# Performance work log

Measured on AMD Instinct MI355X. Metric: run time of the kernel, lower is better.

The kernel has to match this reference:

```python
import jax, jax.numpy as jnp
import numpy as np

B, D_IN, H, LAT = 4096, 4096, 4096, 512


def setup_inputs() -> dict:
    key = jax.random.key(0)
    ks = jax.random.split(key, 10)
    s = lambda fan_in: 1.0 / np.sqrt(fan_in)
    return {
        "x": jax.random.normal(ks[0], (B, D_IN), jnp.float32),
        "W_e1": jax.random.normal(ks[1], (D_IN, H), jnp.float32) * s(D_IN),
        "b_e1": jax.random.uniform(ks[2], (H,), jnp.float32),
        "W_e2": jax.random.normal(ks[3], (H, 2 * LAT), jnp.float32) * s(H),
        "b_e2": jax.random.uniform(ks[4], (2 * LAT,), jnp.float32),
        "W_d1": jax.random.normal(ks[5], (LAT, H), jnp.float32) * s(LAT),
        "b_d1": jax.random.uniform(ks[6], (H,), jnp.float32),
        "W_d2": jax.random.normal(ks[7], (H, D_IN), jnp.float32) * s(H),
        "b_d2": jax.random.uniform(ks[8], (D_IN,), jnp.float32),
        "eps": jax.random.normal(ks[9], (B, LAT), jnp.float32),
    }


def reference(x, W_e1, b_e1, W_e2, b_e2, W_d1, b_d1, W_d2, b_d2, eps):
    # encoder MLP
    h = jax.nn.relu(x @ W_e1 + b_e1)
    z = h @ W_e2 + b_e2                      # [B, 2*LAT]
    mu, logvar = z[:, :LAT], z[:, LAT:]
    # reparameterize: cholesky(diag(exp(logvar))) @ eps + mu == exp(0.5*logvar)*eps + mu
    zs = mu + jnp.exp(0.5 * logvar) * eps    # [B, LAT]
    # decoder MLP
    hd = jax.nn.relu(zs @ W_d1 + b_d1)
    recon = hd @ W_d2 + b_d2                 # [B, D_IN]
    return recon, mu, logvar
```

## Files before the change

### kernel.cpp

```cpp
#include <hip/hip_runtime.h>
#include <hip/hip_bf16.h>

typedef __attribute__((ext_vector_type(8))) __bf16 bf16x8;
typedef __attribute__((ext_vector_type(4))) float f32x4;
typedef __attribute__((ext_vector_type(4))) unsigned short ushort4v;
typedef unsigned short u16;

__device__ __forceinline__ u16 f2bf_bits(float f) {
    union { float f; unsigned int u; } x; x.f = f;
    unsigned int r = x.u + 0x7FFFu + ((x.u >> 16) & 1u);
    return (u16)(r >> 16);
}

__device__ __forceinline__ void gload_lds16(const void* g, void* l) {
    __builtin_amdgcn_global_load_lds(
        (const __attribute__((address_space(1))) void*)g,
        (__attribute__((address_space(3))) void*)l, 16, 0, 0);
}

#define BARRIER()  __builtin_amdgcn_s_barrier()
#define LGKM0()    asm volatile("s_waitcnt lgkmcnt(0)" ::: "memory")
#define VMW8()     asm volatile("s_waitcnt vmcnt(8)" ::: "memory")

__global__ void cvt4(const float* __restrict__ in, u16* __restrict__ out, int n) {
    int i = (blockIdx.x * 256 + threadIdx.x) << 2;
    if (i >= n) return;
    f32x4 v = *reinterpret_cast<const f32x4*>(in + i);
    ushort4v o;
    o.x = f2bf_bits(v.x); o.y = f2bf_bits(v.y);
    o.z = f2bf_bits(v.z); o.w = f2bf_bits(v.w);
    *reinterpret_cast<ushort4v*>(out + i) = o;
}

__global__ __launch_bounds__(256)
void transpose_cvt64(const float* __restrict__ in, u16* __restrict__ out,
                     int R, int C) {
    __shared__ float t[64][67];
    const int c0 = blockIdx.x << 6;
    const int r0 = blockIdx.y << 6;
    const int tx = threadIdx.x & 15;
    const int ty = threadIdx.x >> 4;
    #pragma unroll
    for (int j = 0; j < 4; ++j) {
        f32x4 v = *reinterpret_cast<const f32x4*>(
            &in[(size_t)(r0 + ty + 16 * j) * C + c0 + (tx << 2)]);
        *reinterpret_cast<f32x4*>(&t[ty + 16 * j][tx << 2]) = v;
    }
    __syncthreads();
    const int oc = threadIdx.x >> 2;
    const int rr = (threadIdx.x & 3) << 2;
    #pragma unroll
    for (int j = 0; j < 4; ++j) {
        const int r = rr + 16 * j;
        ushort4v o;
        o.x = f2bf_bits(t[r + 0][oc]);
        o.y = f2bf_bits(t[r + 1][oc]);
        o.z = f2bf_bits(t[r + 2][oc]);
        o.w = f2bf_bits(t[r + 3][oc]);
        *reinterpret_cast<ushort4v*>(&out[(size_t)(c0 + oc) * R + r0 + r]) = o;
    }
}

__global__ __launch_bounds__(256)
void zred(const float* __restrict__ P, const float* __restrict__ be2,
          const float* __restrict__ eps, float* __restrict__ mu,
          float* __restrict__ lv, u16* __restrict__ zs) {
    const int i = blockIdx.x * 256 + threadIdx.x;
    const int r = i >> 7;
    const int c4 = (i & 127) << 2;
    const size_t base = (size_t)r * 1024 + c4;
    const size_t PS = (size_t)4096 * 1024;

    f32x4 m = *reinterpret_cast<const f32x4*>(P + base);
    f32x4 l = *reinterpret_cast<const f32x4*>(P + base + 512);
    #pragma unroll
    for (int s = 1; s < 4; ++s) {
        m += *reinterpret_cast<const f32x4*>(P + s * PS + base);
        l += *reinterpret_cast<const f32x4*>(P + s * PS + base + 512);
    }
    m += *reinterpret_cast<const f32x4*>(be2 + c4);
    l += *reinterpret_cast<const f32x4*>(be2 + 512 + c4);

    const size_t ob = (size_t)r * 512 + c4;
    *reinterpret_cast<f32x4*>(mu + ob) = m;
    *reinterpret_cast<f32x4*>(lv + ob) = l;

    f32x4 e = *reinterpret_cast<const f32x4*>(eps + ob);
    ushort4v o;
    o.x = f2bf_bits(m.x + __expf(0.5f * l.x) * e.x);
    o.y = f2bf_bits(m.y + __expf(0.5f * l.y) * e.y);
    o.z = f2bf_bits(m.z + __expf(0.5f * l.z) * e.z);
    o.w = f2bf_bits(m.w + __expf(0.5f * l.w) * e.w);
    *reinterpret_cast<ushort4v*>(zs + ob) = o;
}

template<int MODE>
__global__ __launch_bounds__(512, 2)
void gemm256(const u16* __restrict__ A, const u16* __restrict__ Bt,
             const float* __restrict__ bias,
             u16* __restrict__ obf, float* __restrict__ of32,
             int M, int N, int K, int ntiles)
{
    extern __shared__ char lds[];
    const int tid  = threadIdx.x;
    const int lane = tid & 63;
    const int w    = tid >> 6;
    const int wr   = w >> 2;
    const int wc   = w & 3;

    int bid = blockIdx.x;
    int sid = 0;
    int nwg = gridDim.x;
    if (MODE == 3) { sid = bid & 3; bid >>= 2; nwg >>= 2; }
    const int cpx = nwg >> 3;
    bid = (bid & 7) * cpx + (bid >> 3);
    const int nbx  = N >> 8;
    const int brow = (bid / nbx) << 8;
    const int bcol = (bid % nbx) << 8;
    const int kbase = (MODE == 3) ? sid * ntiles : 0;
    float* pout = (MODE == 3) ? of32 + (size_t)sid * M * N : of32;

    const int srow  = tid >> 3;
    const int scole = (((tid & 7) ^ (srow & 7)) << 4) >> 1;
    const size_t aoff = (size_t)(brow + srow) * K + scole;
    const size_t boff = (size_t)(bcol + srow) * K + scole;
    const size_t rowK64 = (size_t)64 * K;
    const int wave1024 = w << 10;

    const int lo16 = (lane >> 4) << 4;
    const int swzm = (lane & 7) << 4;
    const int low0 = lo16 ^ swzm;
    const int low1 = (64 | lo16) ^ swzm;
    const int rA   = (lane & 15) << 7;
    const int rB   = ((((wc & 1) << 6) | (lane & 15)) << 7);
    const int regA = wr << 14;
    const int regB = 32768 + ((wc >> 1) << 14);

    bf16x8 a[4][2];
    bf16x8 b0[2][2];
    bf16x8 b1[2][2];
    f32x4 acc[8][4];
    #pragma unroll
    for (int m = 0; m < 8; ++m)
        #pragma unroll
        for (int n = 0; n < 4; ++n)
            acc[m][n] = (f32x4)(0.0f);

#define STAGE_A(buf, h, kt) do { \
    const u16* _s = A + aoff + (size_t)(h) * 128 * K + (size_t)(kt) * 64; \
    gload_lds16(_s,          lds + ((buf) << 16) + ((h) << 14) + wave1024); \
    gload_lds16(_s + rowK64, lds + ((buf) << 16) + ((h) << 14) + 8192 + wave1024); \
} while (0)

#define STAGE_B(buf, h, kt) do { \
    const u16* _s = Bt + boff + (size_t)(h) * 128 * K + (size_t)(kt) * 64; \
    gload_lds16(_s,          lds + ((buf) << 16) + 32768 + ((h) << 14) + wave1024); \
    gload_lds16(_s + rowK64, lds + ((buf) << 16) + 32768 + ((h) << 14) + 8192 + wave1024); \
} while (0)

#define READ_A(buf, g) do { \
    _Pragma("unroll") \
    for (int m = 0; m < 4; ++m) { \
        const int _b = ((buf) << 16) + regA + rA + ((((g) << 2) + m) << 11); \
        a[m][0] = *reinterpret_cast<const bf16x8*>(lds + _b + low0); \
        a[m][1] = *reinterpret_cast<const bf16x8*>(lds + _b + low1); \
    } \
} while (0)

#define READ_B0(buf) do { \
    _Pragma("unroll") \
    for (int n = 0; n < 2; ++n) { \
        const int _b = ((buf) << 16) + regB + rB + (n << 11); \
        b0[n][0] = *reinterpret_cast<const bf16x8*>(lds + _b + low0); \
        b0[n][1] = *reinterpret_cast<const bf16x8*>(lds + _b + low1); \
    } \
} while (0)

#define READ_B1(buf) do { \
    _Pragma("unroll") \
    for (int n = 0; n < 2; ++n) { \
        const int _b = ((buf) << 16) + regB + rB + ((n + 2) << 11); \
        b1[n][0] = *reinterpret_cast<const bf16x8*>(lds + _b + low0); \
        b1[n][1] = *reinterpret_cast<const bf16x8*>(lds + _b + low1); \
    } \
} while (0)

#define MM(bx, mb, nb) do { \
    __builtin_amdgcn_s_setprio(1); \
    _Pragma("unroll") \
    for (int m = 0; m < 4; ++m) \
        _Pragma("unroll") \
        for (int n = 0; n < 2; ++n) \
            _Pragma("unroll") \
            for (int s = 0; s < 2; ++s) \
                acc[(mb) + m][(nb) + n] = __builtin_amdgcn_mfma_f32_16x16x32_bf16( \
                    a[m][s], bx[n][s], acc[(mb) + m][(nb) + n], 0, 0, 0); \
    __builtin_amdgcn_s_setprio(0); \
} while (0)

    const int NIT = ntiles >> 1;

    STAGE_A(0, 0, kbase); STAGE_A(0, 1, kbase); STAGE_B(0, 0, kbase); STAGE_B(0, 1, kbase);
    STAGE_A(1, 0, kbase + 1); STAGE_A(1, 1, kbase + 1); STAGE_B(1, 0, kbase + 1); STAGE_B(1, 1, kbase + 1);
    VMW8(); BARRIER();
    READ_A(0, 0); READ_B0(0);

    for (int it = 0; it < NIT; ++it) {
        const int tn0r = 2 * it + 2;
        const int tn1r = 2 * it + 3;
        const int tn0 = kbase + (tn0r < ntiles ? tn0r : ntiles - 1);
        const int tn1 = kbase + (tn1r < ntiles ? tn1r : ntiles - 1);

        BARRIER(); LGKM0();
        MM(b0, 0, 0);
        READ_B1(0);

        BARRIER(); LGKM0();
        STAGE_B(0, 0, tn0);
        MM(b1, 0, 2);
        READ_A(0, 1);

        BARRIER(); LGKM0();
        STAGE_B(0, 1, tn0);
        MM(b1, 4, 2);

        BARRIER(); LGKM0();
        STAGE_A(0, 0, tn0); STAGE_A(0, 1, tn0);
        MM(b0, 4, 0);
        VMW8();
        READ_A(1, 0); READ_B0(1);

        BARRIER(); LGKM0();
        MM(b0, 0, 0);
        READ_B1(1);

        BARRIER(); LGKM0();
        STAGE_B(1, 0, tn1);
        MM(b1, 0, 2);
        READ_A(1, 1);

        BARRIER(); LGKM0();
        STAGE_B(1, 1, tn1);
        MM(b1, 4, 2);

        BARRIER(); LGKM0();
        STAGE_A(1, 0, tn1); STAGE_A(1, 1, tn1);
        MM(b0, 4, 0);
        VMW8();
        READ_A(0, 0); READ_B0(0);
    }

    float bb[4];
    #pragma unroll
    for (int n = 0; n < 4; ++n)
        bb[n] = (MODE == 3) ? 0.0f : bias[bcol + (wc << 6) + (n << 4) + (lane & 15)];

    const int erow0 = brow + (wr << 7) + ((lane >> 4) << 2);
    const int ecol0 = bcol + (wc << 6) + (lane & 15);

    #pragma unroll
    for (int m = 0; m < 8; ++m) {
        #pragma unroll
        for (int i = 0; i < 4; ++i) {
            const int r = erow0 + (m << 4) + i;
            #pragma unroll
            for (int n = 0; n < 4; ++n) {
                const int c = ecol0 + (n << 4);
                float v = acc[m][n][i] + bb[n];
                if (MODE == 0) {
                    v = v > 0.0f ? v : 0.0f;
                    obf[(size_t)r * N + c] = f2bf_bits(v);
                } else {
                    pout[(size_t)r * N + c] = v;
                }
            }
        }
    }
#undef STAGE_A
#undef STAGE_B
#undef READ_A
#undef READ_B0
#undef READ_B1
#undef MM
}

extern "C" void kernel_launch(void* const* d_in, const int* in_sizes, int n_in,
                              void* d_out, int out_size, void* d_ws, size_t ws_size,
                              hipStream_t stream) {
    const float* x   = (const float*)d_in[0];
    const float* We1 = (const float*)d_in[1];
    const float* be1 = (const float*)d_in[2];
    const float* We2 = (const float*)d_in[3];
    const float* be2 = (const float*)d_in[4];
    const float* Wd1 = (const float*)d_in[5];
    const float* bd1 = (const float*)d_in[6];
    const float* Wd2 = (const float*)d_in[7];
    const float* bd2 = (const float*)d_in[8];
    const float* eps = (const float*)d_in[9];

    const int B = 4096, D = 4096, H = 4096, LAT = 512;

    char* ws = (char*)d_ws;
    u16*   xb   = (u16*)(ws);
    u16*   w1t  = (u16*)(ws + 33554432);
    u16*   w2t  = (u16*)(ws + 67108864);
    u16*   w3t  = (u16*)(ws + 75497472);
    u16*   w4t  = (u16*)(ws + 79691776);
    u16*   h    = (u16*)(ws + 113246208);
    float* part = (float*)(ws);
    u16*   zs   = (u16*)(ws + 113246208);
    u16*   hd   = (u16*)(ws);

    float* recon = (float*)d_out;
    float* mu    = recon + (size_t)B * D;
    float* lv    = mu + (size_t)B * LAT;

    hipFuncSetAttribute(reinterpret_cast<const void*>(gemm256<0>),
                        hipFuncAttributeMaxDynamicSharedMemorySize, 131072);
    hipFuncSetAttribute(reinterpret_cast<const void*>(gemm256<1>),
                        hipFuncAttributeMaxDynamicSharedMemorySize, 131072);
    hipFuncSetAttribute(reinterpret_cast<const void*>(gemm256<3>),
                        hipFuncAttributeMaxDynamicSharedMemorySize, 131072);

    cvt4<<<(B * D / 4 + 255) / 256, 256, 0, stream>>>(x, xb, B * D);
    transpose_cvt64<<<dim3(H / 64, D / 64), 256, 0, stream>>>(We1, w1t, D, H);
    transpose_cvt64<<<dim3(2 * LAT / 64, H / 64), 256, 0, stream>>>(We2, w2t, H, 2 * LAT);
    transpose_cvt64<<<dim3(H / 64, LAT / 64), 256, 0, stream>>>(Wd1, w3t, LAT, H);
    transpose_cvt64<<<dim3(D / 64, H / 64), 256, 0, stream>>>(Wd2, w4t, H, D);

    gemm256<0><<<(B / 256) * (H / 256), 512, 131072, stream>>>(
        xb, w1t, be1, h, nullptr, B, H, D, D / 64);
    gemm256<3><<<(B / 256) * (2 * LAT / 256) * 4, 512, 131072, stream>>>(
        h, w2t, nullptr, nullptr, part, B, 2 * LAT, H, (H / 64) / 4);
    zred<<<(B * LAT / 4) / 256, 256, 0, stream>>>(part, be2, eps, mu, lv, zs);
    gemm256<0><<<(B / 256) * (H / 256), 512, 131072, stream>>>(
        zs, w3t, bd1, hd, nullptr, B, H, LAT, LAT / 64);
    gemm256<1><<<(B / 256) * (D / 256), 512, 131072, stream>>>(
        hd, w4t, bd2, nullptr, recon, B, D, H, H / 64);
}
```

Measured before the change: 371.9 us.

## Switch GEMM core to 32x32x16 MFMA and widen transpose stores

Replaces the 16x16x32 bf16 MFMA tiling with 32x32x16 MFMA, which changes the LDS fragment read layout, the accumulator shape and the epilogue row/column mapping. Larger MFMA tiles reuse each operand fragment across more output, which cuts LDS read traffic and instruction count per FLOP. The transpose-convert kernel also now writes 16-byte bf16 vectors instead of 8-byte ones. The cost is a different LDS bank access pattern and larger per-instruction latency that the existing schedule must hide.

```diff
diff --git a/kernel.cpp b/kernel.cpp
--- a/kernel.cpp
+++ b/kernel.cpp
@@ -3,7 +3,9 @@
 
 typedef __attribute__((ext_vector_type(8))) __bf16 bf16x8;
 typedef __attribute__((ext_vector_type(4))) float f32x4;
+typedef __attribute__((ext_vector_type(16))) float f32x16;
 typedef __attribute__((ext_vector_type(4))) unsigned short ushort4v;
+typedef __attribute__((ext_vector_type(8))) unsigned short ushort8v;
 typedef unsigned short u16;
 
 __device__ __forceinline__ u16 f2bf_bits(float f) {
@@ -47,17 +49,16 @@
         *reinterpret_cast<f32x4*>(&t[ty + 16 * j][tx << 2]) = v;
     }
     __syncthreads();
-    const int oc = threadIdx.x >> 2;
-    const int rr = (threadIdx.x & 3) << 2;
-    #pragma unroll
-    for (int j = 0; j < 4; ++j) {
-        const int r = rr + 16 * j;
-        ushort4v o;
-        o.x = f2bf_bits(t[r + 0][oc]);
-        o.y = f2bf_bits(t[r + 1][oc]);
-        o.z = f2bf_bits(t[r + 2][oc]);
-        o.w = f2bf_bits(t[r + 3][oc]);
-        *reinterpret_cast<ushort4v*>(&out[(size_t)(c0 + oc) * R + r0 + r]) = o;
+    const int orow8 = threadIdx.x >> 3;
+    const int seg8  = (threadIdx.x & 7) << 3;
+    #pragma unroll
+    for (int p = 0; p < 2; ++p) {
+        const int oc = orow8 + (p << 5);
+        ushort8v o;
+        #pragma unroll
+        for (int i = 0; i < 8; ++i)
+            o[i] = f2bf_bits(t[seg8 + i][oc]);
+        *reinterpret_cast<ushort8v*>(&out[(size_t)(c0 + oc) * R + r0 + seg8]) = o;
     }
 }
 
@@ -127,24 +128,22 @@
     const size_t rowK64 = (size_t)64 * K;
     const int wave1024 = w << 10;
 
-    const int lo16 = (lane >> 4) << 4;
     const int swzm = (lane & 7) << 4;
-    const int low0 = lo16 ^ swzm;
-    const int low1 = (64 | lo16) ^ swzm;
-    const int rA   = (lane & 15) << 7;
-    const int rB   = ((((wc & 1) << 6) | (lane & 15)) << 7);
+    const int kA   = (lane >> 5) << 4;
+    const int rA32 = (lane & 31) << 7;
     const int regA = wr << 14;
     const int regB = 32768 + ((wc >> 1) << 14);
-
-    bf16x8 a[4][2];
-    bf16x8 b0[2][2];
-    bf16x8 b1[2][2];
-    f32x4 acc[8][4];
-    #pragma unroll
-    for (int m = 0; m < 8; ++m)
+    const int rB32 = (wc & 1) << 13;
+
+    bf16x8 aa[2][4];
+    bf16x8 b0f[4];
+    bf16x8 b1f[4];
+    f32x16 acc[4][2];
+    #pragma unroll
+    for (int mt = 0; mt < 4; ++mt)
         #pragma unroll
-        for (int n = 0; n < 4; ++n)
-            acc[m][n] = (f32x4)(0.0f);
+        for (int nt = 0; nt < 2; ++nt)
+            acc[mt][nt] = (f32x16)(0.0f);
 
 #define STAGE_A(buf, h, kt) do { \
     const u16* _s = A + aoff + (size_t)(h) * 128 * K + (size_t)(kt) * 64; \
@@ -158,43 +157,33 @@
     gload_lds16(_s + rowK64, lds + ((buf) << 16) + 32768 + ((h) << 14) + 8192 + wave1024); \
 } while (0)
 
-#define READ_A(buf, g) do { \
+#define READ_A32(buf, g) do { \
     _Pragma("unroll") \
-    for (int m = 0; m < 4; ++m) { \
-        const int _b = ((buf) << 16) + regA + rA + ((((g) << 2) + m) << 11); \
-        a[m][0] = *reinterpret_cast<const bf16x8*>(lds + _b + low0); \
-        a[m][1] = *reinterpret_cast<const bf16x8*>(lds + _b + low1); \
+    for (int mt = 0; mt < 2; ++mt) { \
+        const int _b = ((buf) << 16) + regA + ((((g) << 1) + mt) << 12) + rA32; \
+        _Pragma("unroll") \
+        for (int s = 0; s < 4; ++s) \
+            aa[mt][s] = *reinterpret_cast<const bf16x8*>( \
+                lds + _b + ((((s) << 5) | kA) ^ swzm)); \
     } \
 } while (0)
 
-#define READ_B0(buf) do { \
+#define READ_B32(buf, bf, nt) do { \
+    const int _b = ((buf) << 16) + regB + rB32 + ((nt) << 12) + ((lane & 31) << 7); \
     _Pragma("unroll") \
-    for (int n = 0; n < 2; ++n) { \
-        const int _b = ((buf) << 16) + regB + rB + (n << 11); \
-        b0[n][0] = *reinterpret_cast<const bf16x8*>(lds + _b + low0); \
-        b0[n][1] = *reinterpret_cast<const bf16x8*>(lds + _b + low1); \
-    } \
-} while (0)
-
-#define READ_B1(buf) do { \
-    _Pragma("unroll") \
-    for (int n = 0; n < 2; ++n) { \
-        const int _b = ((buf) << 16) + regB + rB + ((n + 2) << 11); \
-        b1[n][0] = *reinterpret_cast<const bf16x8*>(lds + _b + low0); \
-        b1[n][1] = *reinterpret_cast<const bf16x8*>(lds + _b + low1); \
-    } \
-} while (0)
-
-#define MM(bx, mb, nb) do { \
+    for (int s = 0; s < 4; ++s) \
+        bf[s] = *reinterpret_cast<const bf16x8*>( \
+            lds + _b + ((((s) << 5) | kA) ^ swzm)); \
+} while (0)
+
+#define MM32(bf, g, nt) do { \
     __builtin_amdgcn_s_setprio(1); \
     _Pragma("unroll") \
-    for (int m = 0; m < 4; ++m) \
+    for (int s = 0; s < 4; ++s) \
         _Pragma("unroll") \
-        for (int n = 0; n < 2; ++n) \
-            _Pragma("unroll") \
-            for (int s = 0; s < 2; ++s) \
-                acc[(mb) + m][(nb) + n] = __builtin_amdgcn_mfma_f32_16x16x32_bf16( \
-                    a[m][s], bx[n][s], acc[(mb) + m][(nb) + n], 0, 0, 0); \
+        for (int mt = 0; mt < 2; ++mt) \
+            acc[((g) << 1) + mt][nt] = __builtin_amdgcn_mfma_f32_32x32x16_bf16( \
+                aa[mt][s], bf[s], acc[((g) << 1) + mt][nt], 0, 0, 0); \
     __builtin_amdgcn_s_setprio(0); \
 } while (0)
 
@@ -203,7 +192,7 @@
     STAGE_A(0, 0, kbase); STAGE_A(0, 1, kbase); STAGE_B(0, 0, kbase); STAGE_B(0, 1, kbase);
     STAGE_A(1, 0, kbase + 1); STAGE_A(1, 1, kbase + 1); STAGE_B(1, 0, kbase + 1); STAGE_B(1, 1, kbase + 1);
     VMW8(); BARRIER();
-    READ_A(0, 0); READ_B0(0);
+    READ_A32(0, 0); READ_B32(0, b0f, 0);
 
     for (int it = 0; it < NIT; ++it) {
         const int tn0r = 2 * it + 2;
@@ -212,76 +201,76 @@
         const int tn1 = kbase + (tn1r < ntiles ? tn1r : ntiles - 1);
 
         BARRIER(); LGKM0();
-        MM(b0, 0, 0);
-        READ_B1(0);
+        MM32(b0f, 0, 0);
+        READ_B32(0, b1f, 1);
 
         BARRIER(); LGKM0();
         STAGE_B(0, 0, tn0);
-        MM(b1, 0, 2);
-        READ_A(0, 1);
+        MM32(b1f, 0, 1);
+        READ_A32(0, 1);
 
         BARRIER(); LGKM0();
         STAGE_B(0, 1, tn0);
-        MM(b1, 4, 2);
+        MM32(b1f, 1, 1);
 
         BARRIER(); LGKM0();
         STAGE_A(0, 0, tn0); STAGE_A(0, 1, tn0);
-        MM(b0, 4, 0);
+        MM32(b0f, 1, 0);
         VMW8();
-        READ_A(1, 0); READ_B0(1);
-
-        BARRIER(); LGKM0();
-        MM(b0, 0, 0);
-        READ_B1(1);
+        READ_A32(1, 0); READ_B32(1, b0f, 0);
+
+        BARRIER(); LGKM0();
+        MM32(b0f, 0, 0);
+        READ_B32(1, b1f, 1);
 
         BARRIER(); LGKM0();
         STAGE_B(1, 0, tn1);
-        MM(b1, 0, 2);
-        READ_A(1, 1);
+        MM32(b1f, 0, 1);
+        READ_A32(1, 1);
 
         BARRIER(); LGKM0();
         STAGE_B(1, 1, tn1);
-        MM(b1, 4, 2);
+        MM32(b1f, 1, 1);
 
         BARRIER(); LGKM0();
         STAGE_A(1, 0, tn1); STAGE_A(1, 1, tn1);
-        MM(b0, 4, 0);
+        MM32(b0f, 1, 0);
         VMW8();
-        READ_A(0, 0); READ_B0(0);
-    }
-
-    float bb[4];
-    #pragma unroll
-    for (int n = 0; n < 4; ++n)
-        bb[n] = (MODE == 3) ? 0.0f : bias[bcol + (wc << 6) + (n << 4) + (lane & 15)];
-
-    const int erow0 = brow + (wr << 7) + ((lane >> 4) << 2);
-    const int ecol0 = bcol + (wc << 6) + (lane & 15);
-
-    #pragma unroll
-    for (int m = 0; m < 8; ++m) {
+        READ_A32(0, 0); READ_B32(0, b0f, 0);
+    }
+
+    float bb2[2];
+    #pragma unroll
+    for (int nt = 0; nt < 2; ++nt)
+        bb2[nt] = (MODE == 3) ? 0.0f
+                              : bias[bcol + (wc << 6) + (nt << 5) + (lane & 31)];
+
+    const int erow = brow + (wr << 7) + ((lane >> 5) << 2);
+    const int ecol = bcol + (wc << 6) + (lane & 31);
+
+    #pragma unroll
+    for (int mt = 0; mt < 4; ++mt) {
         #pragma unroll
-        for (int i = 0; i < 4; ++i) {
-            const int r = erow0 + (m << 4) + i;
+        for (int r = 0; r < 16; ++r) {
+            const int row = erow + (mt << 5) + (r & 3) + ((r >> 2) << 3);
             #pragma unroll
-            for (int n = 0; n < 4; ++n) {
-                const int c = ecol0 + (n << 4);
-                float v = acc[m][n][i] + bb[n];
+            for (int nt = 0; nt < 2; ++nt) {
+                const int c = ecol + (nt << 5);
+                float v = acc[mt][nt][r] + bb2[nt];
                 if (MODE == 0) {
                     v = v > 0.0f ? v : 0.0f;
-                    obf[(size_t)r * N + c] = f2bf_bits(v);
+                    obf[(size_t)row * N + c] = f2bf_bits(v);
                 } else {
-                    pout[(size_t)r * N + c] = v;
+                    pout[(size_t)row * N + c] = v;
                 }
             }
         }
     }
 #undef STAGE_A
 #undef STAGE_B
-#undef READ_A
-#undef READ_B0
-#undef READ_B1
-#undef MM
+#undef READ_A32
+#undef READ_B32
+#undef MM32
 }
 
 extern "C" void kernel_launch(void* const* d_in, const int* in_sizes, int n_in,
```

Result: slower. 400.1 us (+7.6%).
